# Performance work log

Hardware: AMD Instinct MI355X
Metric: run time of the kernel (lower is better)

The kernel has to match this reference:

```python
import jax, jax.numpy as jnp
import numpy as np
from jax import lax

INT8_NARROW = (-127.0, 127.0)   # brevitas Int8WeightPerTensorFloat (narrow range)
INT8_FULL = (-128.0, 127.0)     # brevitas Int8ActPerTensorFloat
INT32 = (-2.0**31, 2.0**31 - 1)


def _fake_quant(v, scale, qmin, qmax):
    # round-to-nearest, clip, dequant (per-tensor)
    return jnp.clip(jnp.round(v / scale), qmin, qmax) * scale


def _conv(x, w, stride):
    return lax.conv_general_dilated(
        x, w, window_strides=(stride, stride), padding=[(1, 1), (1, 1)],
        dimension_numbers=("NCHW", "OIHW", "NCHW"))


def setup_inputs() -> dict:
    key = jax.random.key(0)
    ks = jax.random.split(key, 5)
    B, Cin, Cout, H = 64, 256, 512, 28
    x = jax.random.normal(ks[0], (B, Cin, H, H), dtype=jnp.float32)
    w1 = jax.random.normal(ks[1], (Cout, Cin, 3, 3), dtype=jnp.float32) * 0.05
    b1 = jax.random.normal(ks[2], (Cout,), dtype=jnp.float32) * 0.01
    w2 = jax.random.normal(ks[3], (Cout, Cout, 3, 3), dtype=jnp.float32) * 0.05
    b2 = jax.random.normal(ks[4], (Cout,), dtype=jnp.float32) * 0.01
    return {
        "x": x, "w1": w1, "b1": b1, "w2": w2, "b2": b2,
        "in_scale": jnp.full((1,), 0.05, dtype=jnp.float32),
        "act1_scale": jnp.full((1,), 0.05, dtype=jnp.float32),
        "act2_scale": jnp.full((1,), 0.05, dtype=jnp.float32),
    }


def reference(x, w1, b1, w2, b2, in_scale, act1_scale, act2_scale):
    s_in = in_scale[0]
    s_a1 = act1_scale[0]
    s_a2 = act2_scale[0]

    # conv1: per-tensor int8 weight fake-quant (max-abs stats, narrow range)
    s_w1 = jnp.max(jnp.abs(w1)) / 127.0
    wq1 = _fake_quant(w1, s_w1, *INT8_NARROW)
    bq1 = _fake_quant(b1, s_in * s_w1, *INT32)  # Int32Bias: scale = in_scale*w_scale
    out = _conv(x, wq1, 2) + bq1[None, :, None, None]

    # act1: int8 activation fake-quant (learned per-tensor scale)
    out = _fake_quant(out, s_a1, *INT8_FULL)

    # conv2
    s_w2 = jnp.max(jnp.abs(w2)) / 127.0
    wq2 = _fake_quant(w2, s_w2, *INT8_NARROW)
    bq2 = _fake_quant(b2, s_a1 * s_w2, *INT32)
    out = _conv(out, wq2, 1) + bq2[None, :, None, None]

    # act2
    out = _fake_quant(out, s_a2, *INT8_FULL)
    return out
```

## Files before the change

kernel.cpp:

```cpp
#include <hip/hip_runtime.h>

typedef int i32x4 __attribute__((ext_vector_type(4)));

__device__ __forceinline__ void gl_lds16(const signed char* g, signed char* l) {
    __builtin_amdgcn_global_load_lds(
        (const __attribute__((address_space(1))) void*)g,
        (__attribute__((address_space(3))) void*)l, 16, 0, 0);
}

__device__ __forceinline__ unsigned lds_addr(const signed char* p) {
    return (unsigned)(uintptr_t)(const __attribute__((address_space(3))) signed char*)p;
}

__device__ __forceinline__ i32x4 lds_read_b128a(unsigned a) {
    i32x4 r;
    asm volatile("ds_read_b128 %0, %1" : "=v"(r) : "v"(a));
    return r;
}

#define XQ_SCALE 2048.0f
#define XQ_DELTA (1.0f / 2048.0f)

__device__ __forceinline__ float block_max256(const float* __restrict__ part, int base,
                                              float* __restrict__ sred) {
    float m = part[base + (threadIdx.x & 255)];
#pragma unroll
    for (int off = 32; off > 0; off >>= 1)
        m = fmaxf(m, __shfl_down(m, off));
    __syncthreads();
    if ((threadIdx.x & 63) == 0) sred[threadIdx.x >> 6] = m;
    __syncthreads();
    return fmaxf(fmaxf(sred[0], sred[1]), fmaxf(sred[2], sred[3]));
}

__global__ __launch_bounds__(256) void fused_pre_kernel(
    const float* __restrict__ x,
    const float* __restrict__ w1, const float* __restrict__ w2,
    float* __restrict__ part,
    signed char* __restrict__ xhi, signed char* __restrict__ xlo,
    signed char* __restrict__ act) {
    __shared__ float t[128][33];
    __shared__ float sred[4];
    const int blk = blockIdx.x;
    const int tid = threadIdx.x;
    const uint4 z = {0, 0, 0, 0};

    if (blk < 512) {
        const bool second = blk >= 256;
        const float* w = second ? w2 : w1;
        const int n4 = second ? 589824 : 294912;
        float m = 0.0f;
        for (int i = (blk & 255) * 256 + tid; i < n4; i += 65536) {
            float4 v = ((const float4*)w)[i];
            m = fmaxf(m, fmaxf(fmaxf(fabsf(v.x), fabsf(v.y)), fmaxf(fabsf(v.z), fabsf(v.w))));
        }
#pragma unroll
        for (int off = 32; off > 0; off >>= 1)
            m = fmaxf(m, __shfl_down(m, off));
        if ((tid & 63) == 0) sred[tid >> 6] = m;
        __syncthreads();
        if (tid == 0)
            part[blk] = fmaxf(fmaxf(sred[0], sred[1]), fmaxf(sred[2], sred[3]));
    } else if (blk < 976) {
        const int thr = (blk - 512) * 256 + tid;
        const int b = thr / (116 * 16);
        const int rr = thr - b * (116 * 16);
        const int p = rr >> 4;
        const int ch = rr & 15;
        int h, w;
        if (p < 30)      { h = 0;          w = p; }
        else if (p < 60) { h = 29;         w = p - 30; }
        else if (p < 88) { h = p - 60 + 1; w = 0; }
        else             { h = p - 88 + 1; w = 29; }
        const int off = (b * 900 + h * 30 + w) * 256 + ch * 16;
        *(uint4*)(xhi + off) = z;
        *(uint4*)(xlo + off) = z;
    } else if (blk < 1456) {
        const int thr = (blk - 976) * 256 + tid;
        const int b = thr / (60 * 32);
        const int rr = thr - b * (60 * 32);
        const int p = rr >> 5;
        const int ch = rr & 31;
        int h, w;
        if (p < 16)      { h = 0;          w = p; }
        else if (p < 32) { h = 15;         w = p - 16; }
        else if (p < 46) { h = p - 32 + 1; w = 0; }
        else             { h = p - 46 + 1; w = 15; }
        const int off = (b * 256 + h * 16 + w) * 512 + ch * 16;
        *(uint4*)(act + off) = z;
    } else {
        const int xb = blk - 1456;
        const int hwb = xb % 25;
        const int rest = xb / 25;
        const int cb = rest & 1;
        const int b = rest >> 1;
        const int c0 = cb * 128;
        const int hw0 = hwb * 32;
#pragma unroll
        for (int ci = 0; ci < 4; ++ci) {
            const int crow = (tid >> 3) + ci * 32;
            const int hwo = (tid & 7) * 4;
            const int hw = hw0 + hwo;
            if (hw < 784) {
                const float4 v = *(const float4*)&x[(b * 256 + c0 + crow) * 784 + hw];
                t[crow][hwo + 0] = v.x;
                t[crow][hwo + 1] = v.y;
                t[crow][hwo + 2] = v.z;
                t[crow][hwo + 3] = v.w;
            }
        }
        __syncthreads();
        const int hw_l = tid >> 3;
        const int cg = (tid & 7) * 16;
        const int hw = hw0 + hw_l;
        if (hw < 784) {
            union { signed char c[16]; uint4 u; } ph, pl;
#pragma unroll
            for (int j = 0; j < 16; ++j) {
                const float v = t[cg + j][hw_l];
                int q = (int)rintf(v * XQ_SCALE);
                q = max(-16383, min(16383, q));
                ph.c[j] = (signed char)(q >> 7);
                pl.c[j] = (signed char)(q & 127);
            }
            const int r = hw / 28;
            const int o = (b * 900 + (r + 1) * 30 + (hw - r * 28) + 1) * 256 + c0 + cg;
            *(uint4*)&xhi[o] = ph.u;
            *(uint4*)&xlo[o] = pl.u;
        }
    }
}

__global__ __launch_bounds__(256) void prep_w_kernel(
    const float* __restrict__ w1, const float* __restrict__ w2,
    const float* __restrict__ b1, const float* __restrict__ b2,
    const float* __restrict__ part,
    const float* __restrict__ in_scale, const float* __restrict__ act1_scale,
    signed char* __restrict__ wq1, signed char* __restrict__ wq2,
    float* __restrict__ bq1, float* __restrict__ bq2,
    float* __restrict__ wmax) {
    __shared__ __align__(16) signed char sw[4608];
    __shared__ float sred[4];
    const int blk = blockIdx.x;
    const int tid = threadIdx.x;

    if (blk < 512) {
        const float inv_s = 127.0f / block_max256(part, 0, sred);
        const int n = blk;
        const float4* src = (const float4*)(w1 + n * 2304);
#pragma unroll
        for (int rd = 0; rd < 3; ++rd) {
            const int f = rd * 256 + tid;
            if (f < 576) {
                const float4 v = src[f];
                float q0 = fminf(fmaxf(rintf(v.x * inv_s), -127.0f), 127.0f);
                float q1 = fminf(fmaxf(rintf(v.y * inv_s), -127.0f), 127.0f);
                float q2 = fminf(fmaxf(rintf(v.z * inv_s), -127.0f), 127.0f);
                float q3 = fminf(fmaxf(rintf(v.w * inv_s), -127.0f), 127.0f);
                const int i0 = f * 4;
                int cin, r;
                cin = i0 / 9;       r = i0 - cin * 9;       sw[r * 256 + cin] = (signed char)(int)q0;
                cin = (i0+1) / 9;   r = (i0+1) - cin * 9;   sw[r * 256 + cin] = (signed char)(int)q1;
                cin = (i0+2) / 9;   r = (i0+2) - cin * 9;   sw[r * 256 + cin] = (signed char)(int)q2;
                cin = (i0+3) / 9;   r = (i0+3) - cin * 9;   sw[r * 256 + cin] = (signed char)(int)q3;
            }
        }
        __syncthreads();
        if (tid < 144) *(uint4*)&wq1[n * 2304 + tid * 16] = *(const uint4*)&sw[tid * 16];
    } else if (blk < 1024) {
        const float inv_s = 127.0f / block_max256(part, 256, sred);
        const int n = blk - 512;
        const float4* src = (const float4*)(w2 + n * 4608);
#pragma unroll
        for (int rd = 0; rd < 5; ++rd) {
            const int f = rd * 256 + tid;
            if (f < 1152) {
                const float4 v = src[f];
                float q0 = fminf(fmaxf(rintf(v.x * inv_s), -127.0f), 127.0f);
                float q1 = fminf(fmaxf(rintf(v.y * inv_s), -127.0f), 127.0f);
                float q2 = fminf(fmaxf(rintf(v.z * inv_s), -127.0f), 127.0f);
                float q3 = fminf(fmaxf(rintf(v.w * inv_s), -127.0f), 127.0f);
                const int i0 = f * 4;
                int cin, r;
                cin = i0 / 9;       r = i0 - cin * 9;       sw[r * 512 + cin] = (signed char)(int)q0;
                cin = (i0+1) / 9;   r = (i0+1) - cin * 9;   sw[r * 512 + cin] = (signed char)(int)q1;
                cin = (i0+2) / 9;   r = (i0+2) - cin * 9;   sw[r * 512 + cin] = (signed char)(int)q2;
                cin = (i0+3) / 9;   r = (i0+3) - cin * 9;   sw[r * 512 + cin] = (signed char)(int)q3;
            }
        }
        __syncthreads();
        for (int o = tid; o < 288; o += 256)
            *(uint4*)&wq2[n * 4608 + o * 16] = *(const uint4*)&sw[o * 16];
    } else {
        const float m1 = block_max256(part, 0, sred);
        const float m2 = block_max256(part, 256, sred);
        if (tid == 0) { wmax[0] = m1; wmax[1] = m2; }
        for (int idx = tid; idx < 1024; idx += 256) {
            if (idx < 512) {
                const float s = (*in_scale) * (m1 * (1.0f / 127.0f));
                float q = rintf(b1[idx] / s);
                q = fminf(fmaxf(q, -2147483648.0f), 2147483648.0f);
                bq1[idx] = q * s;
            } else {
                const int j = idx - 512;
                const float s = (*act1_scale) * (m2 * (1.0f / 127.0f));
                float q = rintf(b2[j] / s);
                q = fminf(fmaxf(q, -2147483648.0f), 2147483648.0f);
                bq2[j] = q * s;
            }
        }
    }
}

template<int CIN, int STRIDE, int HP, int HOUT, bool SPLIT, bool FINAL>
__global__ __launch_bounds__(256, SPLIT ? 2 : 3) void conv_gemm_kernel(
    const signed char* __restrict__ Ahi,
    const signed char* __restrict__ Alo,
    const signed char* __restrict__ Wt,
    const float* __restrict__ bias,
    const float* __restrict__ wmax,
    const float* __restrict__ s_pre,
    const float* __restrict__ s_act,
    signed char* __restrict__ act_out,
    float* __restrict__ out_final)
{
    constexpr int K = 9 * CIN;
    constexpr int HW = HOUT * HOUT;
    constexpr int NIT = K / 128;
    constexpr int NC = SPLIT ? 8 : 6;
    constexpr int BUFSZ = SPLIT ? 32768 : 24576;
    constexpr int NB = SPLIT ? 4 : 2;

    __shared__ __align__(16) signed char smem[2 * BUFSZ];

    const int tid = threadIdx.x;
    const int lane = tid & 63;
    const int wv = tid >> 6;
    const int pair = wv >> 1;
    const int nh = wv & 1;
    const int quad = lane >> 4;
    const int l16 = lane & 15;
    const int m0 = blockIdx.y * 64;
    const int n0 = blockIdx.x * 128;

    const int lrow = lane >> 3;
    const int koff = ((lane & 7) ^ lrow) * 16;

    const signed char* srcb[NC];
    int dsto[NC];
    bool isA[NC];
    if constexpr (SPLIT) {
#pragma unroll
        for (int i = 0; i < NC; ++i) {
            const int g = wv * 8 + i;
            const int type = g >> 3;
            if (type >= 2) {
                const int c = g - 16;
                srcb[i] = Wt + (n0 + c * 8 + lrow) * K + koff;
                dsto[i] = 16384 + c * 1024;
                isA[i] = false;
            } else {
                const int c = g & 7;
                const int m = m0 + c * 8 + lrow;
                const int b = m / HW;
                const int rem = m - b * HW;
                const int oh = rem / HOUT;
                const int ow = rem - oh * HOUT;
                const int off = ((b * HP + oh * STRIDE) * HP + ow * STRIDE) * CIN + koff;
                srcb[i] = (type == 0 ? Ahi : Alo) + off;
                dsto[i] = type * 8192 + c * 1024;
                isA[i] = true;
            }
        }
    } else {
#pragma unroll
        for (int i = 0; i < NC; ++i) {
            const int g = wv * 6 + i;
            if (g < 8) {
                const int c = g;
                const int m = m0 + c * 8 + lrow;
                const int b = m / HW;
                const int rem = m - b * HW;
                const int oh = rem / HOUT;
                const int ow = rem - oh * HOUT;
                const int off = ((b * HP + oh * STRIDE) * HP + ow * STRIDE) * CIN + koff;
                srcb[i] = Ahi + off;
                dsto[i] = c * 1024;
                isA[i] = true;
            } else {
                const int c = g - 8;
                srcb[i] = Wt + (n0 + c * 8 + lrow) * K + koff;
                dsto[i] = 8192 + c * 1024;
                isA[i] = false;
            }
        }
    }

    const int aoff0 = SPLIT ? (pair * 8192) : 0;
    const int boff0 = SPLIT ? 16384 : 8192;
    const int nfix  = SPLIT ? (nh * 64) : (wv * 32);

    unsigned aad[2][2][4];
    unsigned bad[2][2][NB];
#pragma unroll
    for (int bi = 0; bi < 2; ++bi)
#pragma unroll
        for (int ks = 0; ks < 2; ++ks) {
#pragma unroll
            for (int mi = 0; mi < 4; ++mi) {
                const int row = mi * 16 + l16;
                const int sl = ((ks * 4 + quad) ^ (row & 7)) * 16;
                aad[bi][ks][mi] = lds_addr(&smem[bi * BUFSZ + aoff0 + row * 128 + sl]);
            }
#pragma unroll
            for (int ni = 0; ni < NB; ++ni) {
                const int row = nfix + ni * 16 + l16;
                const int sl = ((ks * 4 + quad) ^ (row & 7)) * 16;
                bad[bi][ks][ni] = lds_addr(&smem[bi * BUFSZ + boff0 + row * 128 + sl]);
            }
        }

    i32x4 acc[4][NB];
#pragma unroll
    for (int mi = 0; mi < 4; ++mi)
#pragma unroll
        for (int ni = 0; ni < NB; ++ni)
            acc[mi][ni] = i32x4{0, 0, 0, 0};

    auto STAGE = [&](int bo, int it) {
        const int k0 = it * 128;
        const int r9 = k0 / CIN;
        const int kh = r9 / 3;
        const int kw = r9 - kh * 3;
        const int ashift = (kh * HP + kw) * CIN + (k0 & (CIN - 1));
#pragma unroll
        for (int i = 0; i < NC; ++i)
            gl_lds16(srcb[i] + (isA[i] ? ashift : k0), &smem[bo + dsto[i]]);
    };

    i32x4 af[2][4], bf[2][NB];

    auto LOADFRAGS = [&](int bi) {
#pragma unroll
        for (int ks = 0; ks < 2; ++ks) {
#pragma unroll
            for (int mi = 0; mi < 4; ++mi)
                af[ks][mi] = lds_read_b128a(aad[bi][ks][mi]);
#pragma unroll
            for (int ni = 0; ni < NB; ++ni)
                bf[ks][ni] = lds_read_b128a(bad[bi][ks][ni]);
        }
    };

    auto MFMAS_KS = [&](int ks) {
        __builtin_amdgcn_s_setprio(1);
#pragma unroll
        for (int mi = 0; mi < 4; ++mi)
#pragma unroll
            for (int ni = 0; ni < NB; ++ni)
                acc[mi][ni] = __builtin_amdgcn_mfma_i32_16x16x64_i8(af[ks][mi], bf[ks][ni], acc[mi][ni], 0, 0, 0);
        __builtin_amdgcn_s_setprio(0);
    };

    auto WAIT_NC = [&]() {
        if constexpr (SPLIT) asm volatile("s_waitcnt vmcnt(8)" ::: "memory");
        else                 asm volatile("s_waitcnt vmcnt(6)" ::: "memory");
    };
    auto LGKM_HALF = [&]() {
        if constexpr (SPLIT) asm volatile("s_waitcnt lgkmcnt(8)" ::: "memory");
        else                 asm volatile("s_waitcnt lgkmcnt(6)" ::: "memory");
    };

    STAGE(0, 0);
    STAGE(BUFSZ, 1);

    for (int it = 0; it < NIT - 2; it += 2) {
        WAIT_NC();
        __builtin_amdgcn_s_barrier();
        __builtin_amdgcn_sched_barrier(0);
        LOADFRAGS(0);
        LGKM_HALF();
        __builtin_amdgcn_sched_barrier(0);
        MFMAS_KS(0);
        asm volatile("s_waitcnt lgkmcnt(0)" ::: "memory");
        __builtin_amdgcn_sched_barrier(0);
        __builtin_amdgcn_s_barrier();
        __builtin_amdgcn_sched_barrier(0);
        STAGE(0, it + 2);
        MFMAS_KS(1);

        WAIT_NC();
        __builtin_amdgcn_s_barrier();
        __builtin_amdgcn_sched_barrier(0);
        LOADFRAGS(1);
        LGKM_HALF();
        __builtin_amdgcn_sched_barrier(0);
        MFMAS_KS(0);
        asm volatile("s_waitcnt lgkmcnt(0)" ::: "memory");
        __builtin_amdgcn_sched_barrier(0);
        __builtin_amdgcn_s_barrier();
        __builtin_amdgcn_sched_barrier(0);
        if (it + 3 < NIT) STAGE(BUFSZ, it + 3);
        MFMAS_KS(1);
    }

    WAIT_NC();
    __builtin_amdgcn_s_barrier();
    __builtin_amdgcn_sched_barrier(0);
    LOADFRAGS(0);
    LGKM_HALF();
    __builtin_amdgcn_sched_barrier(0);
    MFMAS_KS(0);
    asm volatile("s_waitcnt lgkmcnt(0)" ::: "memory");
    __builtin_amdgcn_sched_barrier(0);
    MFMAS_KS(1);

    asm volatile("s_waitcnt vmcnt(0)" ::: "memory");
    __builtin_amdgcn_s_barrier();
    __builtin_amdgcn_sched_barrier(0);
    LOADFRAGS(1);
    LGKM_HALF();
    __builtin_amdgcn_sched_barrier(0);
    MFMAS_KS(0);
    asm volatile("s_waitcnt lgkmcnt(0)" ::: "memory");
    __builtin_amdgcn_sched_barrier(0);
    MFMAS_KS(1);

    if constexpr (SPLIT) {
        __syncthreads();
        if (pair == 1) {
#pragma unroll
            for (int mi = 0; mi < 4; ++mi)
#pragma unroll
                for (int ni = 0; ni < 4; ++ni)
                    *(i32x4*)&smem[nh * 16384 + (mi * 4 + ni) * 1024 + lane * 16] = acc[mi][ni];
        }
        __syncthreads();
        if (pair == 1) return;
#pragma unroll
        for (int mi = 0; mi < 4; ++mi)
#pragma unroll
            for (int ni = 0; ni < 4; ++ni) {
                const i32x4 other = *(const i32x4*)&smem[nh * 16384 + (mi * 4 + ni) * 1024 + lane * 16];
                acc[mi][ni] = acc[mi][ni] * 128 + other;
            }
    }

    float alpha = (*wmax) * (1.0f / 127.0f);
    if (FINAL) alpha *= *s_pre;
    if (SPLIT) alpha *= XQ_DELTA;
    const float sact = *s_act;

    float bv[NB];
#pragma unroll
    for (int ni = 0; ni < NB; ++ni)
        bv[ni] = bias[n0 + nfix + ni * 16 + l16];

#pragma unroll
    for (int mi = 0; mi < 4; ++mi) {
#pragma unroll
        for (int i = 0; i < 4; ++i) {
            const int m = m0 + mi * 16 + quad * 4 + i;
            const int b = m / HW;
            const int rem = m - b * HW;
            const int oh = rem / HOUT;
            const int ow = rem - oh * HOUT;
#pragma unroll
            for (int ni = 0; ni < NB; ++ni) {
                const int col = n0 + nfix + ni * 16 + l16;
                const float v = (float)acc[mi][ni][i] * alpha + bv[ni];
                float q = rintf(v / sact);
                q = fminf(fmaxf(q, -128.0f), 127.0f);
                if (FINAL) {
                    out_final[(b * 512 + col) * HW + oh * HOUT + ow] = q * sact;
                } else {
                    act_out[(b * 256 + (oh + 1) * 16 + (ow + 1)) * 512 + col] = (signed char)(int)q;
                }
            }
        }
    }
}

extern "C" void kernel_launch(void* const* d_in, const int* in_sizes, int n_in,
                              void* d_out, int out_size, void* d_ws, size_t ws_size,
                              hipStream_t stream) {
    const float* x  = (const float*)d_in[0];
    const float* w1 = (const float*)d_in[1];
    const float* b1 = (const float*)d_in[2];
    const float* w2 = (const float*)d_in[3];
    const float* b2 = (const float*)d_in[4];
    const float* in_scale   = (const float*)d_in[5];
    const float* act1_scale = (const float*)d_in[6];
    const float* act2_scale = (const float*)d_in[7];
    float* out = (float*)d_out;

    char* ws = (char*)d_ws;
    float* part = (float*)(ws + 0);
    float* wmax = (float*)(ws + 2048);
    float* bq1 = (float*)(ws + 2176);
    float* bq2 = (float*)(ws + 4224);
    signed char* wq1 = (signed char*)(ws + 8192);
    signed char* wq2 = (signed char*)(ws + 1187840);
    signed char* xhi = (signed char*)(ws + 3547136);
    signed char* xlo = (signed char*)(ws + 18292736);
    signed char* act = (signed char*)(ws + 33038336);

    fused_pre_kernel<<<4656, 256, 0, stream>>>(x, w1, w2, part, xhi, xlo, act);

    prep_w_kernel<<<1025, 256, 0, stream>>>(w1, w2, b1, b2, part, in_scale, act1_scale,
                                            wq1, wq2, bq1, bq2, wmax);

    conv_gemm_kernel<256, 2, 30, 14, true, false><<<dim3(4, 196), 256, 0, stream>>>(
        xhi, xlo, wq1, bq1, wmax, act1_scale, act1_scale, act, nullptr);

    conv_gemm_kernel<512, 1, 16, 14, false, true><<<dim3(4, 196), 256, 0, stream>>>(
        act, nullptr, wq2, bq2, wmax + 1, act1_scale, act2_scale, nullptr, out);
}
```

Before: 225.2 us.

## Restructure GEMM main loop to one barrier pair per two stages; drop LDS transpose in x quant

The main int8 MFMA loop now loads fragments for both LDS buffers into separate register sets and waits for all outstanding global loads before each double-iteration. Both stages are refilled together after a single barrier, so there is one sync point per two K-steps instead of two. This removes a barrier per step but stops overlapping the next stage's global loads with the current buffer's compute, and it needs more fragment registers. Separately, the input-quantization blocks read x directly with strided per-channel loads instead of transposing through a shared-memory tile.

```diff
diff --git a/kernel.cpp b/kernel.cpp
--- a/kernel.cpp
+++ b/kernel.cpp
@@ -39,7 +39,6 @@
     float* __restrict__ part,
     signed char* __restrict__ xhi, signed char* __restrict__ xlo,
     signed char* __restrict__ act) {
-    __shared__ float t[128][33];
     __shared__ float sred[4];
     const int blk = blockIdx.x;
     const int tid = threadIdx.x;
@@ -94,37 +93,21 @@
         const int rest = xb / 25;
         const int cb = rest & 1;
         const int b = rest >> 1;
-        const int c0 = cb * 128;
-        const int hw0 = hwb * 32;
-#pragma unroll
-        for (int ci = 0; ci < 4; ++ci) {
-            const int crow = (tid >> 3) + ci * 32;
-            const int hwo = (tid & 7) * 4;
-            const int hw = hw0 + hwo;
-            if (hw < 784) {
-                const float4 v = *(const float4*)&x[(b * 256 + c0 + crow) * 784 + hw];
-                t[crow][hwo + 0] = v.x;
-                t[crow][hwo + 1] = v.y;
-                t[crow][hwo + 2] = v.z;
-                t[crow][hwo + 3] = v.w;
-            }
-        }
-        __syncthreads();
-        const int hw_l = tid >> 3;
-        const int cg = (tid & 7) * 16;
-        const int hw = hw0 + hw_l;
+        const int c0 = cb * 128 + (tid >> 5) * 16;
+        const int hw = hwb * 32 + (tid & 31);
         if (hw < 784) {
+            const float* xp = x + (b * 256 + c0) * 784 + hw;
             union { signed char c[16]; uint4 u; } ph, pl;
 #pragma unroll
             for (int j = 0; j < 16; ++j) {
-                const float v = t[cg + j][hw_l];
+                const float v = xp[j * 784];
                 int q = (int)rintf(v * XQ_SCALE);
                 q = max(-16383, min(16383, q));
                 ph.c[j] = (signed char)(q >> 7);
                 pl.c[j] = (signed char)(q & 127);
             }
             const int r = hw / 28;
-            const int o = (b * 900 + (r + 1) * 30 + (hw - r * 28) + 1) * 256 + c0 + cg;
+            const int o = (b * 900 + (r + 1) * 30 + (hw - r * 28) + 1) * 256 + c0;
             *(uint4*)&xhi[o] = ph.u;
             *(uint4*)&xlo[o] = pl.u;
         }
@@ -338,9 +321,9 @@
             gl_lds16(srcb[i] + (isA[i] ? ashift : k0), &smem[bo + dsto[i]]);
     };
 
-    i32x4 af[2][4], bf[2][NB];
-
-    auto LOADFRAGS = [&](int bi) {
+    i32x4 af0[2][4], bf0[2][NB], af1[2][4], bf1[2][NB];
+
+    auto LOADF = [&](int bi, i32x4 (&af)[2][4], i32x4 (&bf)[2][NB]) {
 #pragma unroll
         for (int ks = 0; ks < 2; ++ks) {
 #pragma unroll
@@ -352,7 +335,7 @@
         }
     };
 
-    auto MFMAS_KS = [&](int ks) {
+    auto MFMAS = [&](i32x4 (&af)[2][4], i32x4 (&bf)[2][NB], int ks) {
         __builtin_amdgcn_s_setprio(1);
 #pragma unroll
         for (int mi = 0; mi < 4; ++mi)
@@ -362,69 +345,43 @@
         __builtin_amdgcn_s_setprio(0);
     };
 
-    auto WAIT_NC = [&]() {
-        if constexpr (SPLIT) asm volatile("s_waitcnt vmcnt(8)" ::: "memory");
-        else                 asm volatile("s_waitcnt vmcnt(6)" ::: "memory");
-    };
-    auto LGKM_HALF = [&]() {
+    auto LGKM_H = [&]() {
         if constexpr (SPLIT) asm volatile("s_waitcnt lgkmcnt(8)" ::: "memory");
         else                 asm volatile("s_waitcnt lgkmcnt(6)" ::: "memory");
     };
+    auto LGKM_RD = [&]() {
+        if constexpr (SPLIT) asm volatile("s_waitcnt lgkmcnt(15)" ::: "memory");
+        else                 asm volatile("s_waitcnt lgkmcnt(12)" ::: "memory");
+    };
 
     STAGE(0, 0);
     STAGE(BUFSZ, 1);
 
-    for (int it = 0; it < NIT - 2; it += 2) {
-        WAIT_NC();
+    for (int it = 0; it < NIT; it += 2) {
+        asm volatile("s_waitcnt vmcnt(0)" ::: "memory");
         __builtin_amdgcn_s_barrier();
         __builtin_amdgcn_sched_barrier(0);
-        LOADFRAGS(0);
-        LGKM_HALF();
-        __builtin_amdgcn_sched_barrier(0);
-        MFMAS_KS(0);
+        LOADF(0, af0, bf0);
+        LGKM_H();
+        __builtin_amdgcn_sched_barrier(0);
+        MFMAS(af0, bf0, 0);
+        LOADF(1, af1, bf1);
+        LGKM_RD();
+        __builtin_amdgcn_sched_barrier(0);
+        MFMAS(af0, bf0, 1);
+        LGKM_H();
+        __builtin_amdgcn_sched_barrier(0);
+        MFMAS(af1, bf1, 0);
         asm volatile("s_waitcnt lgkmcnt(0)" ::: "memory");
         __builtin_amdgcn_sched_barrier(0);
         __builtin_amdgcn_s_barrier();
         __builtin_amdgcn_sched_barrier(0);
-        STAGE(0, it + 2);
-        MFMAS_KS(1);
-
-        WAIT_NC();
-        __builtin_amdgcn_s_barrier();
-        __builtin_amdgcn_sched_barrier(0);
-        LOADFRAGS(1);
-        LGKM_HALF();
-        __builtin_amdgcn_sched_barrier(0);
-        MFMAS_KS(0);
-        asm volatile("s_waitcnt lgkmcnt(0)" ::: "memory");
-        __builtin_amdgcn_sched_barrier(0);
-        __builtin_amdgcn_s_barrier();
-        __builtin_amdgcn_sched_barrier(0);
-        if (it + 3 < NIT) STAGE(BUFSZ, it + 3);
-        MFMAS_KS(1);
-    }
-
-    WAIT_NC();
-    __builtin_amdgcn_s_barrier();
-    __builtin_amdgcn_sched_barrier(0);
-    LOADFRAGS(0);
-    LGKM_HALF();
-    __builtin_amdgcn_sched_barrier(0);
-    MFMAS_KS(0);
-    asm volatile("s_waitcnt lgkmcnt(0)" ::: "memory");
-    __builtin_amdgcn_sched_barrier(0);
-    MFMAS_KS(1);
-
-    asm volatile("s_waitcnt vmcnt(0)" ::: "memory");
-    __builtin_amdgcn_s_barrier();
-    __builtin_amdgcn_sched_barrier(0);
-    LOADFRAGS(1);
-    LGKM_HALF();
-    __builtin_amdgcn_sched_barrier(0);
-    MFMAS_KS(0);
-    asm volatile("s_waitcnt lgkmcnt(0)" ::: "memory");
-    __builtin_amdgcn_sched_barrier(0);
-    MFMAS_KS(1);
+        if (it + 2 < NIT) {
+            STAGE(0, it + 2);
+            STAGE(BUFSZ, it + 3);
+        }
+        MFMAS(af1, bf1, 1);
+    }
 
     if constexpr (SPLIT) {
         __syncthreads();
```

Result: slower. 233.1 us (+3.5%).
